# Kernel optimization log

Hardware: AMD Instinct MI355X
Metric: run time of the kernel (lower is better)

The kernel has to match this reference:

```python
import jax, jax.numpy as jnp
import numpy as np

EMBED_DIM = 256
NUM_HEADS = 8
HEAD_DIM = EMBED_DIM // NUM_HEADS
WINDOW = 31
B, S = 4, 2048


def _make_params(key):
    ks = jax.random.split(key, 8)
    sc = 0.05
    Wq = jax.random.normal(ks[0], (NUM_HEADS, EMBED_DIM, HEAD_DIM), jnp.float32) * sc
    bq = jax.random.normal(ks[1], (NUM_HEADS, HEAD_DIM), jnp.float32) * sc
    Wk = jax.random.normal(ks[2], (NUM_HEADS, EMBED_DIM, HEAD_DIM), jnp.float32) * sc
    bk = jax.random.normal(ks[3], (NUM_HEADS, HEAD_DIM), jnp.float32) * sc
    Wv = jax.random.normal(ks[4], (NUM_HEADS, EMBED_DIM, HEAD_DIM), jnp.float32) * sc
    bv = jax.random.normal(ks[5], (NUM_HEADS, HEAD_DIM), jnp.float32) * sc
    Wo = jax.random.normal(ks[6], (NUM_HEADS * HEAD_DIM, EMBED_DIM), jnp.float32) * sc
    bo = jax.random.normal(ks[7], (EMBED_DIM,), jnp.float32) * sc
    return Wq, bq, Wk, bk, Wv, bv, Wo, bo


def setup_inputs() -> dict:
    key = jax.random.key(0)
    k1, k2, k3, k4 = jax.random.split(key, 4)
    eeg = jax.random.normal(k1, (B, S, EMBED_DIM), jnp.float32)
    pps = jax.random.normal(k2, (B, S, EMBED_DIM), jnp.float32)
    e2p = _make_params(k3)
    p2e = _make_params(k4)
    names = ["Wq", "bq", "Wk", "bk", "Wv", "bv", "Wo", "bo"]
    inp = {"eeg": eeg, "pps": pps}
    for n, p in zip(names, e2p):
        inp["e2p_" + n] = p
    for n, p in zip(names, p2e):
        inp["p2e_" + n] = p
    return inp


def _cross_window_attn(q_seq, kv_seq, Wq, bq, Wk, bk, Wv, bv, Wo, bo, window):
    # q_seq, kv_seq: [B, S, D]. Each query position i attends to window of
    # the zero-padded kv sequence centered at i (pad positions get bias-only k/v,
    # matching torch Linear applied to zero vectors).
    b, s, d_in = q_seq.shape
    h, _, hd = Wq.shape
    pad = (window - 1) // 2
    kv_pad = jnp.pad(kv_seq, ((0, 0), (pad, pad), (0, 0)))
    Q = jnp.einsum('bsd,hde->bhse', q_seq, Wq) + bq[None, :, None, :]
    K = jnp.einsum('bsd,hde->bhse', kv_pad, Wk) + bk[None, :, None, :]
    V = jnp.einsum('bsd,hde->bhse', kv_pad, Wv) + bv[None, :, None, :]
    idx = jnp.arange(s)[:, None] + jnp.arange(window)[None, :]  # [S, W]
    Kw = K[:, :, idx, :]  # [B, H, S, W, hd]
    Vw = V[:, :, idx, :]
    scores = jnp.einsum('bhse,bhswe->bhsw', Q, Kw) / np.sqrt(hd).astype(np.float32)
    attn = jax.nn.softmax(scores, axis=-1)
    out = jnp.einsum('bhsw,bhswe->bhse', attn, Vw)  # [B, H, S, hd]
    out = out.transpose(0, 2, 1, 3).reshape(b, s, h * hd)
    return out @ Wo + bo


def reference(eeg, pps,
              e2p_Wq, e2p_bq, e2p_Wk, e2p_bk, e2p_Wv, e2p_bv, e2p_Wo, e2p_bo,
              p2e_Wq, p2e_bq, p2e_Wk, p2e_bk, p2e_Wv, p2e_bv, p2e_Wo, p2e_bo):
    fused_eeg = _cross_window_attn(eeg, pps, e2p_Wq, e2p_bq, e2p_Wk, e2p_bk,
                                   e2p_Wv, e2p_bv, e2p_Wo, e2p_bo, WINDOW)
    fused_pps = _cross_window_attn(pps, eeg, p2e_Wq, p2e_bq, p2e_Wk, p2e_bk,
                                   p2e_Wv, p2e_bv, p2e_Wo, p2e_bo, WINDOW)
    return fused_eeg, fused_pps
```

## Files before the change

### kernel.cpp

```cpp
#include <hip/hip_runtime.h>

static __device__ __forceinline__ float bf2f(unsigned short u) {
    return __uint_as_float(((unsigned int)u) << 16);
}
static __device__ __forceinline__ unsigned short f2bf(float f) {
    unsigned int x = __float_as_uint(f);
    unsigned int lsb = (x >> 16) & 1u;
    x += 0x7fffu + lsb;
    return (unsigned short)(x >> 16);
}

typedef __attribute__((ext_vector_type(8))) short short8;
typedef __attribute__((ext_vector_type(4))) float floatx4;

static __device__ __forceinline__ short8 ldg8(const unsigned short* p) {
    short8 v; __builtin_memcpy(&v, p, 16); return v;
}

__global__ __launch_bounds__(256) void repack_kernel(
    const float* e2p_Wq, const float* e2p_bq,
    const float* e2p_Wk, const float* e2p_bk,
    const float* e2p_Wv, const float* e2p_bv,
    const float* e2p_Wo, const float* e2p_bo,
    const float* p2e_Wq, const float* p2e_bq,
    const float* p2e_Wk, const float* p2e_bk,
    const float* p2e_Wv, const float* p2e_bv,
    const float* p2e_Wo, const float* p2e_bo,
    const float* eeg, const float* pps,
    unsigned short* Wpack, unsigned short* Wopack, float* bias_pack, float* bias2,
    unsigned short* Abf)
{
    int idx = blockIdx.x * 256 + threadIdx.x;
    const int WP = 2 * 768 * 256;
    if (idx < WP) {
        int inp = idx / (768 * 256);
        int rem = idx % (768 * 256);
        int n = rem / 256, k = rem % 256;
        int proj = n / 256, h = (n % 256) / 32, e = n % 32;
        const float* W;
        if (inp == 0) W = (proj == 0) ? e2p_Wq : (proj == 1) ? p2e_Wk : p2e_Wv;
        else          W = (proj == 0) ? p2e_Wq : (proj == 1) ? e2p_Wk : e2p_Wv;
        Wpack[idx] = f2bf(W[h * 8192 + k * 32 + e]);
    }
    int idx2 = idx - WP;
    if (idx2 >= 0 && idx2 < 2 * 65536) {
        int dir = idx2 / 65536, rem2 = idx2 % 65536;
        int n = rem2 / 256, k = rem2 % 256;
        Wopack[idx2] = f2bf((dir == 0 ? e2p_Wo : p2e_Wo)[k * 256 + n]);
    }
    if (idx < 1536) {
        int inp = idx / 768, n = idx % 768;
        int proj = n / 256, he = n % 256;
        const float* bsrc;
        if (inp == 0) bsrc = (proj == 0) ? e2p_bq : (proj == 1) ? p2e_bk : p2e_bv;
        else          bsrc = (proj == 0) ? p2e_bq : (proj == 1) ? e2p_bk : e2p_bv;
        bias_pack[idx] = bsrc[he];
    }
    if (idx >= 1536 && idx < 2048) {
        int j = idx - 1536;
        int dir = j / 256, n = j % 256;
        bias2[j] = (dir == 0 ? e2p_bo : p2e_bo)[n];
    }
    {
        long base = (long)idx * 8;
        const float* src = (base < 2097152) ? eeg : pps;
        long off = (base < 2097152) ? base : base - 2097152;
        float v[8];
        __builtin_memcpy(v, src + off, 32);
        unsigned short o[8];
        #pragma unroll
        for (int j = 0; j < 8; ++j) o[j] = f2bf(v[j]);
        __builtin_memcpy(Abf + base, o, 16);
    }
}

template<bool C_F32>
__global__ __launch_bounds__(256) void mfma_gemm_kernel(
    const unsigned short* __restrict__ A0, const unsigned short* __restrict__ A1,
    const unsigned short* __restrict__ B0t, const unsigned short* __restrict__ B1t,
    const float* __restrict__ bias0, const float* __restrict__ bias1,
    void* __restrict__ C0v, void* __restrict__ C1v,
    int N)
{
    __shared__ __align__(16) unsigned short Cs[128][136];

    const int z = blockIdx.z;
    const unsigned short* A = z ? A1 : A0;
    const unsigned short* Bt = z ? B1t : B0t;
    const float* bias = z ? bias1 : bias0;
    void* Cv = z ? C1v : C0v;

    const int tid = threadIdx.x;
    const long m0 = (long)blockIdx.x * 128;
    const int n0 = blockIdx.y * 128;

    const int lane = tid & 63;
    const int wv = tid >> 6;
    const int wm = (wv >> 1) * 64, wn = (wv & 1) * 64;
    const int fr = lane & 15;
    const int fq = (lane >> 4) * 8;

    const unsigned short* Ap = A + (m0 + wm + fr) * 256 + fq;
    const unsigned short* Bp = Bt + (long)(n0 + wn + fr) * 256 + fq;

    floatx4 acc[4][4] = {};
    short8 af[2][4], bf_[2][4];

    #pragma unroll
    for (int i = 0; i < 4; ++i) af[0][i] = ldg8(Ap + i * 4096);
    #pragma unroll
    for (int j = 0; j < 4; ++j) bf_[0][j] = ldg8(Bp + j * 4096);

    #pragma unroll
    for (int kc = 0; kc < 8; ++kc) {
        const int cur = kc & 1, nxt = cur ^ 1;
        if (kc < 7) {
            const int ko = (kc + 1) * 32;
            #pragma unroll
            for (int i = 0; i < 4; ++i) af[nxt][i] = ldg8(Ap + ko + i * 4096);
            #pragma unroll
            for (int j = 0; j < 4; ++j) bf_[nxt][j] = ldg8(Bp + ko + j * 4096);
        }
        #pragma unroll
        for (int i = 0; i < 4; ++i)
            #pragma unroll
            for (int j = 0; j < 4; ++j)
                acc[i][j] = __builtin_amdgcn_mfma_f32_16x16x32_bf16(af[cur][i], bf_[cur][j], acc[i][j], 0, 0, 0);
    }

    float bj[4];
    #pragma unroll
    for (int j = 0; j < 4; ++j) bj[j] = bias[n0 + wn + j * 16 + fr];

    const int cr0 = wm + ((lane >> 4) << 2);
    #pragma unroll
    for (int i = 0; i < 4; ++i)
        #pragma unroll
        for (int j = 0; j < 4; ++j)
            #pragma unroll
            for (int r = 0; r < 4; ++r)
                Cs[cr0 + i * 16 + r][wn + j * 16 + fr] = f2bf(acc[i][j][r] + bj[j]);
    __syncthreads();

    const int rr = tid >> 4, cc = (tid & 15) * 8;
    #pragma unroll
    for (int p = 0; p < 8; ++p) {
        int r = p * 16 + rr;
        unsigned short tmp[8];
        __builtin_memcpy(tmp, &Cs[r][cc], 16);
        if (C_F32) {
            float of[8];
            #pragma unroll
            for (int j = 0; j < 8; ++j) of[j] = bf2f(tmp[j]);
            __builtin_memcpy((float*)Cv + (m0 + r) * N + n0 + cc, of, 32);
        } else {
            __builtin_memcpy((unsigned short*)Cv + (m0 + r) * N + n0 + cc, tmp, 16);
        }
    }
}

#define KROWS 48
#define VROWS 64
#define KVSTR 264
__global__ __launch_bounds__(512) void attn_out_kernel(
    const unsigned short* __restrict__ Y, const float* __restrict__ bias_pack,
    const unsigned short* __restrict__ Wopack, const float* __restrict__ bias2,
    float* __restrict__ out)
{
    __shared__ unsigned short smem[(KROWS + VROWS) * KVSTR];
    unsigned short* Ks = smem;
    unsigned short* Vs = smem + KROWS * KVSTR;
    unsigned short (*Ps)[16][72] = (unsigned short(*)[16][72])smem;
    unsigned short (*As)[KVSTR] = (unsigned short(*)[KVSTR])smem;

    const int s0 = blockIdx.x * 16;
    const int b = blockIdx.y, dir = blockIdx.z;
    const int kvinp = 1 - dir;
    const int tid = threadIdx.x;

    const float* bkv = bias_pack + kvinp * 768;
    const long kvbase = ((long)kvinp * 8192 + b * 2048) * 768;

    {
        const int r = tid >> 3, seg = (tid & 7) * 32;
        int p = s0 - 15 + r;
        unsigned short vr[32];
        if (p >= 0 && p < 2048) {
            __builtin_memcpy(vr, Y + kvbase + (long)p * 768 + 512 + seg, 64);
        } else {
            #pragma unroll
            for (int j = 0; j < 32; ++j) vr[j] = f2bf(bkv[512 + seg + j]);
        }
        __builtin_memcpy(&Vs[r * KVSTR + seg], vr, 64);
        if (tid < 384) {
            unsigned short kr[32];
            if (p >= 0 && p < 2048) {
                __builtin_memcpy(kr, Y + kvbase + (long)p * 768 + 256 + seg, 64);
            } else {
                #pragma unroll
                for (int j = 0; j < 32; ++j) kr[j] = f2bf(bkv[256 + seg + j]);
            }
            __builtin_memcpy(&Ks[r * KVSTR + seg], kr, 64);
        }
    }

    const int lane = tid & 63;
    const int wv = tid >> 6;
    const int fr = lane & 15, q4 = lane >> 4;
    short8 aq = ldg8(Y + ((long)dir * 8192 + b * 2048 + s0 + fr) * 768 + wv * 32 + q4 * 8);

    __syncthreads();

    floatx4 sacc[3] = {};
    #pragma unroll
    for (int kvt = 0; kvt < 3; ++kvt) {
        short8 bk_ = *(const short8*)&Ks[(kvt * 16 + fr) * KVSTR + wv * 32 + q4 * 8];
        sacc[kvt] = __builtin_amdgcn_mfma_f32_16x16x32_bf16(aq, bk_, sacc[kvt], 0, 0, 0);
    }

    float sv[3][4];
    float mx[4] = {-3.0e38f, -3.0e38f, -3.0e38f, -3.0e38f};
    #pragma unroll
    for (int kvt = 0; kvt < 3; ++kvt)
        #pragma unroll
        for (int reg = 0; reg < 4; ++reg) {
            int i = q4 * 4 + reg;
            int jc = kvt * 16 + fr;
            int d = jc - i;
            float x = (d >= 0 && d <= 30) ? sacc[kvt][reg] * 0.17677669529663687f : -3.0e38f;
            sv[kvt][reg] = x;
            mx[reg] = fmaxf(mx[reg], x);
        }
    #pragma unroll
    for (int off = 1; off < 16; off <<= 1)
        #pragma unroll
        for (int reg = 0; reg < 4; ++reg)
            mx[reg] = fmaxf(mx[reg], __shfl_xor(mx[reg], off));
    float ps[4] = {};
    #pragma unroll
    for (int kvt = 0; kvt < 3; ++kvt)
        #pragma unroll
        for (int reg = 0; reg < 4; ++reg) {
            float e = __expf(sv[kvt][reg] - mx[reg]);
            sv[kvt][reg] = e;
            ps[reg] += e;
        }
    #pragma unroll
    for (int off = 1; off < 16; off <<= 1)
        #pragma unroll
        for (int reg = 0; reg < 4; ++reg)
            ps[reg] += __shfl_xor(ps[reg], off);

    __syncthreads();

    #pragma unroll
    for (int reg = 0; reg < 4; ++reg) {
        int i = q4 * 4 + reg;
        #pragma unroll
        for (int kvt = 0; kvt < 3; ++kvt)
            Ps[wv][i][kvt * 16 + fr] = f2bf(sv[kvt][reg]);
        Ps[wv][i][48 + fr] = 0;
    }

    floatx4 oacc[2] = {};
    #pragma unroll
    for (int ch = 0; ch < 2; ++ch) {
        short8 ap = *(const short8*)&Ps[wv][fr][ch * 32 + q4 * 8];
        #pragma unroll
        for (int et = 0; et < 2; ++et) {
            short8 bv;
            #pragma unroll
            for (int j = 0; j < 8; ++j)
                bv[j] = (short)Vs[(ch * 32 + q4 * 8 + j) * KVSTR + wv * 32 + et * 16 + fr];
            oacc[et] = __builtin_amdgcn_mfma_f32_16x16x32_bf16(ap, bv, oacc[et], 0, 0, 0);
        }
    }

    float rs[4];
    #pragma unroll
    for (int reg = 0; reg < 4; ++reg) rs[reg] = 1.0f / ps[reg];

    __syncthreads();

    #pragma unroll
    for (int et = 0; et < 2; ++et)
        #pragma unroll
        for (int reg = 0; reg < 4; ++reg)
            As[q4 * 4 + reg][wv * 32 + et * 16 + fr] = f2bf(oacc[et][reg] * rs[reg]);

    __syncthreads();

    const unsigned short* Wo = Wopack + dir * 65536;
    const int nw = wv * 32;
    floatx4 oa[2] = {};
    #pragma unroll
    for (int kc = 0; kc < 8; ++kc) {
        short8 ap = *(const short8*)&As[fr][kc * 32 + q4 * 8];
        #pragma unroll
        for (int j = 0; j < 2; ++j) {
            short8 bw = ldg8(Wo + (nw + j * 16 + fr) * 256 + kc * 32 + q4 * 8);
            oa[j] = __builtin_amdgcn_mfma_f32_16x16x32_bf16(ap, bw, oa[j], 0, 0, 0);
        }
    }

    float bj[2];
    #pragma unroll
    for (int j = 0; j < 2; ++j) bj[j] = bias2[dir * 256 + nw + j * 16 + fr];

    float* outp = out + (long)dir * 2097152;
    #pragma unroll
    for (int j = 0; j < 2; ++j)
        #pragma unroll
        for (int reg = 0; reg < 4; ++reg) {
            int i = q4 * 4 + reg;
            outp[((long)b * 2048 + s0 + i) * 256 + nw + j * 16 + fr] = oa[j][reg] + bj[j];
        }
}

extern "C" void kernel_launch(void* const* d_in, const int* in_sizes, int n_in,
                              void* d_out, int out_size, void* d_ws, size_t ws_size,
                              hipStream_t stream)
{
    float* out = (float*)d_out;

    char* ws = (char*)d_ws;
    unsigned short* Wpack   = (unsigned short*)(ws + 0);
    unsigned short* Wopack  = (unsigned short*)(ws + 786432);
    float*          biasP   = (float*)(ws + 1048576);
    float*          bias2   = (float*)(ws + 1054720);
    unsigned short* Y       = (unsigned short*)(ws + 1056768);
    unsigned short* Abf     = (unsigned short*)(ws + 26222592);

    repack_kernel<<<2048, 256, 0, stream>>>(
        (const float*)d_in[2],  (const float*)d_in[3],
        (const float*)d_in[4],  (const float*)d_in[5],
        (const float*)d_in[6],  (const float*)d_in[7],
        (const float*)d_in[8],  (const float*)d_in[9],
        (const float*)d_in[10], (const float*)d_in[11],
        (const float*)d_in[12], (const float*)d_in[13],
        (const float*)d_in[14], (const float*)d_in[15],
        (const float*)d_in[16], (const float*)d_in[17],
        (const float*)d_in[0],  (const float*)d_in[1],
        Wpack, Wopack, biasP, bias2, Abf);

    mfma_gemm_kernel<false><<<dim3(64, 6, 2), 256, 0, stream>>>(
        Abf, Abf + 2097152, Wpack, Wpack + 196608, biasP, biasP + 768,
        Y, Y + 8192 * 768, 768);

    attn_out_kernel<<<dim3(128, 4, 2), 512, 0, stream>>>(Y, biasP, Wopack, bias2, out);
}
```

Baseline: 157.8 us.

## Pre-swizzle activations and weights into MFMA fragment order for coalesced loads

The repack kernel now writes the bf16 activations, QKV weights and output-projection weights in a fragment-major layout, where each 16-row by 32-k tile is stored as 64 contiguous lane vectors. The GEMM and the output-projection stage then read operands at lane*8 offsets, so each wavefront load is one contiguous 1 KB chunk instead of 16 rows strided by 512 bytes. The unused fp32-output template path is removed. The repack now does more index arithmetic and its weight reads become strided gathers, but that step handles a small amount of data.

```diff
diff --git a/kernel.cpp b/kernel.cpp
--- a/kernel.cpp
+++ b/kernel.cpp
@@ -16,6 +16,7 @@
 static __device__ __forceinline__ short8 ldg8(const unsigned short* p) {
     short8 v; __builtin_memcpy(&v, p, 16); return v;
 }
+
 
 __global__ __launch_bounds__(256) void repack_kernel(
     const float* e2p_Wq, const float* e2p_bq,
@@ -30,23 +31,31 @@
     unsigned short* Wpack, unsigned short* Wopack, float* bias_pack, float* bias2,
     unsigned short* Abf)
 {
-    int idx = blockIdx.x * 256 + threadIdx.x;
-    const int WP = 2 * 768 * 256;
-    if (idx < WP) {
-        int inp = idx / (768 * 256);
-        int rem = idx % (768 * 256);
-        int n = rem / 256, k = rem % 256;
+    const int idx = blockIdx.x * 256 + threadIdx.x;
+
+    if (idx < 49152) {
+        int inp = idx / 24576, r = idx % 24576;
+        int n = r >> 5, k8 = r & 31;
+        int kc = k8 >> 2, q4 = k8 & 3, kb = k8 * 8;
         int proj = n / 256, h = (n % 256) / 32, e = n % 32;
         const float* W;
         if (inp == 0) W = (proj == 0) ? e2p_Wq : (proj == 1) ? p2e_Wk : p2e_Wv;
         else          W = (proj == 0) ? p2e_Wq : (proj == 1) ? e2p_Wk : e2p_Wv;
-        Wpack[idx] = f2bf(W[h * 8192 + k * 32 + e]);
-    }
-    int idx2 = idx - WP;
-    if (idx2 >= 0 && idx2 < 2 * 65536) {
-        int dir = idx2 / 65536, rem2 = idx2 % 65536;
-        int n = rem2 / 256, k = rem2 % 256;
-        Wopack[idx2] = f2bf((dir == 0 ? e2p_Wo : p2e_Wo)[k * 256 + n]);
+        unsigned short o[8];
+        #pragma unroll
+        for (int j = 0; j < 8; ++j) o[j] = f2bf(W[h * 8192 + (kb + j) * 32 + e]);
+        __builtin_memcpy(Wpack + inp * 196608 + ((n >> 4) * 8 + kc) * 512 + (q4 * 16 + (n & 15)) * 8, o, 16);
+    }
+    int i2 = idx - 49152;
+    if (i2 >= 0 && i2 < 16384) {
+        int dir = i2 / 8192, r = i2 % 8192;
+        int n = r >> 5, k8 = r & 31;
+        int kc = k8 >> 2, q4 = k8 & 3, kb = k8 * 8;
+        const float* Wo = dir ? p2e_Wo : e2p_Wo;
+        unsigned short o[8];
+        #pragma unroll
+        for (int j = 0; j < 8; ++j) o[j] = f2bf(Wo[(kb + j) * 256 + n]);
+        __builtin_memcpy(Wopack + dir * 65536 + ((n >> 4) * 8 + kc) * 512 + (q4 * 16 + (n & 15)) * 8, o, 16);
     }
     if (idx < 1536) {
         int inp = idx / 768, n = idx % 768;
@@ -62,33 +71,34 @@
         bias2[j] = (dir == 0 ? e2p_bo : p2e_bo)[n];
     }
     {
-        long base = (long)idx * 8;
-        const float* src = (base < 2097152) ? eeg : pps;
-        long off = (base < 2097152) ? base : base - 2097152;
+        int m_total = idx >> 5;
+        int k8 = idx & 31;
+        int inp = m_total >> 13, m = m_total & 8191;
+        int kc = k8 >> 2, q4 = k8 & 3, kb = k8 * 8;
+        const float* src = inp ? pps : eeg;
         float v[8];
-        __builtin_memcpy(v, src + off, 32);
+        __builtin_memcpy(v, src + (long)m * 256 + kb, 32);
         unsigned short o[8];
         #pragma unroll
         for (int j = 0; j < 8; ++j) o[j] = f2bf(v[j]);
-        __builtin_memcpy(Abf + base, o, 16);
-    }
-}
-
-template<bool C_F32>
+        __builtin_memcpy(Abf + inp * 2097152 + (((m >> 4) * 8 + kc) * 512 + (q4 * 16 + (m & 15)) * 8), o, 16);
+    }
+}
+
 __global__ __launch_bounds__(256) void mfma_gemm_kernel(
     const unsigned short* __restrict__ A0, const unsigned short* __restrict__ A1,
-    const unsigned short* __restrict__ B0t, const unsigned short* __restrict__ B1t,
+    const unsigned short* __restrict__ B0f, const unsigned short* __restrict__ B1f,
     const float* __restrict__ bias0, const float* __restrict__ bias1,
-    void* __restrict__ C0v, void* __restrict__ C1v,
+    unsigned short* __restrict__ C0, unsigned short* __restrict__ C1,
     int N)
 {
     __shared__ __align__(16) unsigned short Cs[128][136];
 
     const int z = blockIdx.z;
     const unsigned short* A = z ? A1 : A0;
-    const unsigned short* Bt = z ? B1t : B0t;
+    const unsigned short* Bf = z ? B1f : B0f;
     const float* bias = z ? bias1 : bias0;
-    void* Cv = z ? C1v : C0v;
+    unsigned short* C = z ? C1 : C0;
 
     const int tid = threadIdx.x;
     const long m0 = (long)blockIdx.x * 128;
@@ -97,29 +107,27 @@
     const int lane = tid & 63;
     const int wv = tid >> 6;
     const int wm = (wv >> 1) * 64, wn = (wv & 1) * 64;
-    const int fr = lane & 15;
-    const int fq = (lane >> 4) * 8;
-
-    const unsigned short* Ap = A + (m0 + wm + fr) * 256 + fq;
-    const unsigned short* Bp = Bt + (long)(n0 + wn + fr) * 256 + fq;
+    const int fr = lane & 15, q4 = lane >> 4;
+
+    const unsigned short* Aw = A + ((blockIdx.x * 8 + (wm >> 4)) * 8) * 512 + lane * 8;
+    const unsigned short* Bw = Bf + ((blockIdx.y * 8 + (wn >> 4)) * 8) * 512 + lane * 8;
 
     floatx4 acc[4][4] = {};
     short8 af[2][4], bf_[2][4];
 
     #pragma unroll
-    for (int i = 0; i < 4; ++i) af[0][i] = ldg8(Ap + i * 4096);
-    #pragma unroll
-    for (int j = 0; j < 4; ++j) bf_[0][j] = ldg8(Bp + j * 4096);
+    for (int i = 0; i < 4; ++i) af[0][i] = ldg8(Aw + i * 4096);
+    #pragma unroll
+    for (int j = 0; j < 4; ++j) bf_[0][j] = ldg8(Bw + j * 4096);
 
     #pragma unroll
     for (int kc = 0; kc < 8; ++kc) {
         const int cur = kc & 1, nxt = cur ^ 1;
         if (kc < 7) {
-            const int ko = (kc + 1) * 32;
-            #pragma unroll
-            for (int i = 0; i < 4; ++i) af[nxt][i] = ldg8(Ap + ko + i * 4096);
-            #pragma unroll
-            for (int j = 0; j < 4; ++j) bf_[nxt][j] = ldg8(Bp + ko + j * 4096);
+            #pragma unroll
+            for (int i = 0; i < 4; ++i) af[nxt][i] = ldg8(Aw + (i * 8 + kc + 1) * 512);
+            #pragma unroll
+            for (int j = 0; j < 4; ++j) bf_[nxt][j] = ldg8(Bw + (j * 8 + kc + 1) * 512);
         }
         #pragma unroll
         for (int i = 0; i < 4; ++i)
@@ -132,7 +140,7 @@
     #pragma unroll
     for (int j = 0; j < 4; ++j) bj[j] = bias[n0 + wn + j * 16 + fr];
 
-    const int cr0 = wm + ((lane >> 4) << 2);
+    const int cr0 = wm + (q4 << 2);
     #pragma unroll
     for (int i = 0; i < 4; ++i)
         #pragma unroll
@@ -148,14 +156,7 @@
         int r = p * 16 + rr;
         unsigned short tmp[8];
         __builtin_memcpy(tmp, &Cs[r][cc], 16);
-        if (C_F32) {
-            float of[8];
-            #pragma unroll
-            for (int j = 0; j < 8; ++j) of[j] = bf2f(tmp[j]);
-            __builtin_memcpy((float*)Cv + (m0 + r) * N + n0 + cc, of, 32);
-        } else {
-            __builtin_memcpy((unsigned short*)Cv + (m0 + r) * N + n0 + cc, tmp, 16);
-        }
+        __builtin_memcpy(C + (m0 + r) * N + n0 + cc, tmp, 16);
     }
 }
 
@@ -290,7 +291,7 @@
 
     __syncthreads();
 
-    const unsigned short* Wo = Wopack + dir * 65536;
+    const unsigned short* Wo = Wopack + dir * 65536 + lane * 8;
     const int nw = wv * 32;
     floatx4 oa[2] = {};
     #pragma unroll
@@ -298,7 +299,7 @@
         short8 ap = *(const short8*)&As[fr][kc * 32 + q4 * 8];
         #pragma unroll
         for (int j = 0; j < 2; ++j) {
-            short8 bw = ldg8(Wo + (nw + j * 16 + fr) * 256 + kc * 32 + q4 * 8);
+            short8 bw = ldg8(Wo + ((wv * 2 + j) * 8 + kc) * 512);
             oa[j] = __builtin_amdgcn_mfma_f32_16x16x32_bf16(ap, bw, oa[j], 0, 0, 0);
         }
     }
@@ -343,7 +344,7 @@
         (const float*)d_in[0],  (const float*)d_in[1],
         Wpack, Wopack, biasP, bias2, Abf);
 
-    mfma_gemm_kernel<false><<<dim3(64, 6, 2), 256, 0, stream>>>(
+    mfma_gemm_kernel<<<dim3(64, 6, 2), 256, 0, stream>>>(
         Abf, Abf + 2097152, Wpack, Wpack + 196608, biasP, biasP + 768,
         Y, Y + 8192 * 768, 768);
 
```

New measurement: 140.4 us. -11.1%, faster.
